# Kernel tuning notes

Hardware: AMD Instinct MI355X
Metric: run time of the kernel (lower is better)

## Reference

```python
import jax, jax.numpy as jnp
import numpy as np

L, B, D = 4096, 4, 512  # seq_len, batch, embed_dim (nhead=1 so kdim=vdim=D)


def setup_inputs() -> dict:
    key = jax.random.key(0)
    ks = jax.random.split(key, 11)
    sc = 1.0 / np.sqrt(D)
    return {
        "x": jax.random.normal(ks[0], (L, B, D), jnp.float32),
        "e": jax.random.normal(ks[1], (L, B, D), jnp.float32),
        "relay": jax.random.normal(ks[2], (1, B, D), jnp.float32),
        "Wq": jax.random.normal(ks[3], (D, D), jnp.float32) * sc,
        "bq": jax.random.normal(ks[4], (D,), jnp.float32) * sc,
        "Wk": jax.random.normal(ks[5], (D, D), jnp.float32) * sc,
        "bk": jax.random.normal(ks[6], (D,), jnp.float32) * sc,
        "Wv": jax.random.normal(ks[7], (D, D), jnp.float32) * sc,
        "bv": jax.random.normal(ks[8], (D,), jnp.float32) * sc,
        "Wo": jax.random.normal(ks[9], (D, D), jnp.float32) * sc,
        "bo": jax.random.normal(ks[10], (D,), jnp.float32) * sc,
    }


def _window3(t):
    # t: [L,B,D] -> [L,B,3,D] with zero padding at the sequence boundaries
    # (matches nn.Unfold(kernel=[3,1], padding=[1,0]): positions l-1, l, l+1)
    n = t.shape[0]
    tp = jnp.pad(t, ((1, 1), (0, 0), (0, 0)))
    return jnp.stack([tp[:n], tp[1:n + 1], tp[2:n + 2]], axis=2)


def reference(x, e, relay, Wq, bq, Wk, bk, Wv, bv, Wo, bo):
    l, b, d = x.shape
    scale = 1.0 / jnp.sqrt(jnp.asarray(d, x.dtype))

    q = x @ Wq.T + bq          # [L,B,D]
    k = x @ Wk.T + bk
    v = x @ Wv.T + bv

    # cores = [embedding tokens e ; relay broadcast over L]  -> [2,L,B,D]
    s = jnp.broadcast_to(relay, (l, b, d))
    cores = jnp.stack([e, s], axis=0)
    k_c = cores @ Wk.T + bk    # [2,L,B,D]
    v_c = cores @ Wv.T + bv

    # ring (local windowed) attention: window = [k_{l-1},k_l,k_{l+1}, k(e_l), k(relay)]
    kw = jnp.concatenate([_window3(k), jnp.transpose(k_c, (1, 2, 0, 3))], axis=2)  # [L,B,5,D]
    vw = jnp.concatenate([_window3(v), jnp.transpose(v_c, (1, 2, 0, 3))], axis=2)  # [L,B,5,D]
    logits = jnp.einsum('lbd,lbwd->lbw', q, kw) * scale
    alphas = jax.nn.softmax(logits, axis=2)
    ring = jnp.einsum('lbw,lbwd->lbd', alphas, vw)  # [L,B,D]

    # star (relay) attention: query is the UNprojected relay token (as in source)
    k_r = relay @ Wk.T + bk    # [1,B,D]
    v_r = relay @ Wv.T + bv
    kk = jnp.concatenate([k, k_r], axis=0)  # [L+1,B,D]
    vv = jnp.concatenate([v, v_r], axis=0)
    s_logits = jnp.einsum('obd,nbd->bon', relay, kk) * scale  # [B,1,L+1]
    s_alphas = jax.nn.softmax(s_logits, axis=-1)
    star = jnp.einsum('bon,nbd->obd', s_alphas, vv)  # [1,B,D]

    return (ring @ Wo.T + bo, star @ Wo.T + bo)
```

## Files before the change

### kernel.cpp

```cpp
#include <hip/hip_runtime.h>
#include <hip/hip_fp16.h>

#define L_SEQ 4096
#define BATCH 4
#define DIM 512
#define M_ROWS (L_SEQ * BATCH)
#define SCALE 0.04419417382415922f
#define SLS 4097

typedef __attribute__((ext_vector_type(4))) float f32x4;
typedef __attribute__((ext_vector_type(8))) _Float16 f16x8;
typedef __attribute__((ext_vector_type(4))) _Float16 f16x4;

__device__ inline void gload16(const void* g, void* l) {
    __builtin_amdgcn_global_load_lds(
        (const __attribute__((address_space(1))) void*)g,
        (__attribute__((address_space(3))) void*)l, 16, 0, 0);
}

__device__ inline float wred_sum(float s) {
#pragma unroll
    for (int o = 32; o; o >>= 1) s += __shfl_xor(s, o);
    return s;
}
__device__ inline float wred_max(float s) {
#pragma unroll
    for (int o = 32; o; o >>= 1) s = fmaxf(s, __shfl_xor(s, o));
    return s;
}

__global__ __launch_bounds__(256) void prep(
    const float* __restrict__ x, const float* __restrict__ e,
    const float* __restrict__ Wq, const float* __restrict__ Wk,
    const float* __restrict__ Wv, const float* __restrict__ Wo,
    const float* __restrict__ bq, const float* __restrict__ bk, const float* __restrict__ bv,
    const float* __restrict__ relay,
    _Float16* __restrict__ xh, _Float16* __restrict__ eh,
    _Float16* __restrict__ Wqkv, _Float16* __restrict__ Wof, float* __restrict__ bqkv,
    float* __restrict__ krvr, float* __restrict__ star)
{
    const int bid = blockIdx.x;
    if (bid < 16384) {
        size_t i = (size_t)bid * 256 + threadIdx.x;
        const size_t NV = (size_t)M_ROWS * DIM / 4;
        const float* src; _Float16* dst; size_t j;
        if (i < NV) { src = x; dst = xh; j = i; } else { src = e; dst = eh; j = i - NV; }
        float4 v = ((const float4*)src)[j];
        f16x4 h = { (_Float16)v.x, (_Float16)v.y, (_Float16)v.z, (_Float16)v.w };
        ((f16x4*)dst)[j] = h;
    } else if (bid < 19456) {
        int i = (bid - 16384) * 256 + threadIdx.x;
        {
            int r = i >> 9, c = i & 511;
            const float* W = (r < 512) ? Wq : (r < 1024 ? Wk : Wv);
            Wqkv[i] = (_Float16)W[(size_t)(r & 511) * 512 + c];
        }
        if (i < 512 * 512) Wof[i] = (_Float16)Wo[i];
        if (i < 1536) bqkv[i] = (i < 512) ? bq[i] : (i < 1024 ? bk[i - 512] : bv[i - 1024]);
    } else {
        const int o = ((bid - 19456) << 2) + (threadIdx.x >> 6);
        const int lane = threadIdx.x & 63;
        const int sel = o >> 11, rem = o & 2047, b = rem >> 9, j = rem & 511;
        const float* W = sel ? Wv : Wk;
        const float* wr = W + (size_t)j * 512 + lane * 8;
        const float* rp = relay + (size_t)b * 512 + lane * 8;
        float4 w0 = *(const float4*)wr,  w1 = *(const float4*)(wr + 4);
        float4 r0 = *(const float4*)rp,  r1 = *(const float4*)(rp + 4);
        float s = w0.x * r0.x + w0.y * r0.y + w0.z * r0.z + w0.w * r0.w
                + w1.x * r1.x + w1.y * r1.y + w1.z * r1.z + w1.w * r1.w;
        s = wred_sum(s);
        if (lane == 0) {
            krvr[o] = s + (sel ? bv[j] : bk[j]);
            if (o < 2048) star[o] = 0.f;
        }
    }
}

template<int OUT16>
__global__ __launch_bounds__(256) void gemm_bt(
    const _Float16* __restrict__ A, const _Float16* __restrict__ Bm,
    const float* __restrict__ bias, void* __restrict__ Cv,
    int M, int N, int K)
{
    __shared__ _Float16 lA[2][128 * 32];
    __shared__ _Float16 lB[2][128 * 32];
    const int tid = threadIdx.x;
    const int wave = tid >> 6, lane = tid & 63;
    const int row0 = blockIdx.x * 128;
    const int col0 = blockIdx.y * 128;
    const int wm = (wave >> 1) * 64, wn = (wave & 1) * 64;

    f32x4 acc[4][4];
#pragma unroll
    for (int i = 0; i < 4; ++i)
#pragma unroll
        for (int j = 0; j < 4; ++j) acc[i][j] = (f32x4)0.f;

    const int idx0 = tid, idx1 = 256 + tid;
    const int r0_ = idx0 >> 2, c0_ = ((idx0 & 3) ^ ((idx0 >> 3) & 3)) * 8;
    const int r1_ = idx1 >> 2, c1_ = ((idx1 & 3) ^ ((idx1 >> 3) & 3)) * 8;
    const int ldsb0 = (wave * 64) * 8;
    const int ldsb1 = (256 + wave * 64) * 8;

    const int nsteps = K >> 5;
    auto stage = [&](int buf, int t) {
        const int k0 = t << 5;
        gload16(A  + (size_t)(row0 + r0_) * K + k0 + c0_, &lA[buf][ldsb0]);
        gload16(A  + (size_t)(row0 + r1_) * K + k0 + c1_, &lA[buf][ldsb1]);
        gload16(Bm + (size_t)(col0 + r0_) * K + k0 + c0_, &lB[buf][ldsb0]);
        gload16(Bm + (size_t)(col0 + r1_) * K + k0 + c1_, &lB[buf][ldsb1]);
    };
    stage(0, 0);
    stage(1, 1);

    const int rslot = ((lane >> 4) ^ ((lane >> 1) & 3)) * 8;
    const int arb = (wm + (lane & 15)) * 32 + rslot;
    const int brb = (wn + (lane & 15)) * 32 + rslot;

    int cur = 0;
    for (int t = 0; t < nsteps; ++t) {
        if (t + 1 < nsteps) asm volatile("s_waitcnt vmcnt(4)" ::: "memory");
        else                asm volatile("s_waitcnt vmcnt(0)" ::: "memory");
        __builtin_amdgcn_s_barrier();
        f16x8 af[4], bfr[4];
#pragma unroll
        for (int i = 0; i < 4; ++i) af[i]  = *(const f16x8*)(&lA[cur][arb + i * 512]);
#pragma unroll
        for (int i = 0; i < 4; ++i) bfr[i] = *(const f16x8*)(&lB[cur][brb + i * 512]);
        __builtin_amdgcn_s_setprio(1);
#pragma unroll
        for (int mi = 0; mi < 4; ++mi)
#pragma unroll
            for (int ni = 0; ni < 4; ++ni)
                acc[mi][ni] = __builtin_amdgcn_mfma_f32_16x16x32_f16(
                    af[mi], bfr[ni], acc[mi][ni], 0, 0, 0);
        __builtin_amdgcn_s_setprio(0);
        asm volatile("s_waitcnt lgkmcnt(0)" ::: "memory");
        __builtin_amdgcn_s_barrier();
        if (t + 2 < nsteps) stage(cur, t + 2);
        cur ^= 1;
    }

#pragma unroll
    for (int mi = 0; mi < 4; ++mi) {
#pragma unroll
        for (int ni = 0; ni < 4; ++ni) {
            const int col = col0 + wn + ni * 16 + (lane & 15);
            const float bb = bias[col];
#pragma unroll
            for (int r = 0; r < 4; ++r) {
                const int row = row0 + wm + mi * 16 + (lane >> 4) * 4 + r;
                float v = acc[mi][ni][r] + bb;
                if (OUT16) ((_Float16*)Cv)[(size_t)row * N + col] = (_Float16)v;
                else       ((float*)Cv)[(size_t)row * N + col] = v;
            }
        }
    }
}

__global__ __launch_bounds__(256) void ring_attn(
    const _Float16* __restrict__ qkv,
    const _Float16* __restrict__ ekv,
    const float* __restrict__ krvr,
    const float* __restrict__ relay,
    _Float16* __restrict__ ring,
    float* __restrict__ slog)
{
    const int wid = (blockIdx.x << 2) + (threadIdx.x >> 6);
    const int lane = threadIdx.x & 63;
    const int r = wid, b = r & 3, l = r >> 2;
    const int d0 = lane << 3;

    float q[8], rl[8];
    {
        f16x8 t = *(const f16x8*)(qkv + (size_t)r * 1536 + d0);
#pragma unroll
        for (int i = 0; i < 8; ++i) q[i] = (float)t[i];
        const float* rp = relay + (size_t)b * 512 + d0;
        float4 a = *(const float4*)rp, c = *(const float4*)(rp + 4);
        rl[0] = a.x; rl[1] = a.y; rl[2] = a.z; rl[3] = a.w;
        rl[4] = c.x; rl[5] = c.y; rl[6] = c.z; rl[7] = c.w;
    }
    const bool has0 = (l > 0), has2 = (l < L_SEQ - 1);

    auto dotk = [&](const _Float16* kp) -> float {
        f16x8 t = *(const f16x8*)(kp + d0);
        float s = 0.f;
#pragma unroll
        for (int i = 0; i < 8; ++i) s += q[i] * (float)t[i];
        return wred_sum(s);
    };

    float lg[5];
    lg[0] = has0 ? dotk(qkv + (size_t)(r - 4) * 1536 + 512) : 0.f;
    lg[2] = has2 ? dotk(qkv + (size_t)(r + 4) * 1536 + 512) : 0.f;
    lg[3] = dotk(ekv + (size_t)r * 1024);
    {
        f16x8 t = *(const f16x8*)(qkv + (size_t)r * 1536 + 512 + d0);
        float s1 = 0.f, s2 = 0.f;
#pragma unroll
        for (int i = 0; i < 8; ++i) { float kf = (float)t[i]; s1 += q[i] * kf; s2 += rl[i] * kf; }
#pragma unroll
        for (int o = 32; o; o >>= 1) { s1 += __shfl_xor(s1, o); s2 += __shfl_xor(s2, o); }
        lg[1] = s1;
        if (lane == 0) slog[(size_t)b * SLS + l] = s2 * SCALE;
    }
    {
        const float* kp = krvr + (size_t)b * 512 + d0;
        float s = 0.f;
#pragma unroll
        for (int i = 0; i < 8; ++i) s += q[i] * kp[i];
        lg[4] = wred_sum(s);
    }

    float li[5], m = -1e30f;
#pragma unroll
    for (int w = 0; w < 5; ++w) { li[w] = lg[w] * SCALE; m = fmaxf(m, li[w]); }
    float ew[5], Z = 0.f;
#pragma unroll
    for (int w = 0; w < 5; ++w) { ew[w] = expf(li[w] - m); Z += ew[w]; }
    const float inv = 1.f / Z;

    float o8[8] = {0, 0, 0, 0, 0, 0, 0, 0};
    auto addv = [&](const _Float16* vp, float a) {
        f16x8 t = *(const f16x8*)(vp + d0);
#pragma unroll
        for (int i = 0; i < 8; ++i) o8[i] += a * (float)t[i];
    };
    if (has0) addv(qkv + (size_t)(r - 4) * 1536 + 1024, ew[0] * inv);
    addv(qkv + (size_t)r * 1536 + 1024, ew[1] * inv);
    if (has2) addv(qkv + (size_t)(r + 4) * 1536 + 1024, ew[2] * inv);
    addv(ekv + (size_t)r * 1024 + 512, ew[3] * inv);
    {
        const float* vp = krvr + 2048 + (size_t)b * 512 + d0;
        const float a = ew[4] * inv;
#pragma unroll
        for (int i = 0; i < 8; ++i) o8[i] += a * vp[i];
    }
    f16x8 res;
#pragma unroll
    for (int i = 0; i < 8; ++i) res[i] = (_Float16)o8[i];
    *(f16x8*)(ring + (size_t)r * 512 + d0) = res;
}

__global__ __launch_bounds__(1024) void star_softmax(
    const float* __restrict__ relay, const float* __restrict__ krvr,
    float* __restrict__ slog)
{
    const int b = blockIdx.x, t = threadIdx.x, lane = t & 63, w = t >> 6;
    __shared__ float red[16];
    __shared__ float bc[2];
    float* sl = slog + (size_t)b * SLS;

    float p = 0.f;
    if (t < 512) p = relay[(size_t)b * 512 + t] * krvr[(size_t)b * 512 + t];
    p = wred_sum(p);
    if (lane == 0) red[w] = p;
    __syncthreads();
    if (t == 0) { float s = 0.f; for (int i = 0; i < 16; ++i) s += red[i]; bc[0] = s * SCALE; }
    __syncthreads();
    const float selfl = bc[0];
    __syncthreads();

    float v[4];
#pragma unroll
    for (int i = 0; i < 4; ++i) v[i] = sl[t + i * 1024];

    float m = selfl;
#pragma unroll
    for (int i = 0; i < 4; ++i) m = fmaxf(m, v[i]);
    m = wred_max(m);
    if (lane == 0) red[w] = m;
    __syncthreads();
    if (t == 0) { float mm = red[0]; for (int i = 1; i < 16; ++i) mm = fmaxf(mm, red[i]); bc[1] = mm; }
    __syncthreads();
    m = bc[1];

    float ev[4], z = (t == 0) ? expf(selfl - m) : 0.f;
#pragma unroll
    for (int i = 0; i < 4; ++i) { ev[i] = expf(v[i] - m); z += ev[i]; }
    z = wred_sum(z);
    if (lane == 0) red[w] = z;
    __syncthreads();
    if (t == 0) { float s = 0.f; for (int i = 0; i < 16; ++i) s += red[i]; bc[0] = 1.f / s; }
    __syncthreads();
    const float inv = bc[0];

#pragma unroll
    for (int i = 0; i < 4; ++i) sl[t + i * 1024] = ev[i] * inv;
    if (t == 0) sl[SLS - 1] = expf(selfl - m) * inv;
}

__global__ __launch_bounds__(256) void star_out(
    const float* __restrict__ slog, const _Float16* __restrict__ qkv,
    const float* __restrict__ krvr, float* __restrict__ star)
{
    const int b = threadIdx.x >> 6, lane = threadIdx.x & 63;
    const int chunk = blockIdx.x;
    const int d0 = lane << 3;
    const float* al = slog + (size_t)b * SLS;
    float acc[8] = {0, 0, 0, 0, 0, 0, 0, 0};
#pragma unroll 4
    for (int i = 0; i < 64; ++i) {
        const int n = chunk * 64 + i;
        const float a = al[n];
        f16x8 v = *(const f16x8*)(qkv + (size_t)(n * 4 + b) * 1536 + 1024 + d0);
#pragma unroll
        for (int j = 0; j < 8; ++j) acc[j] += a * (float)v[j];
    }
    if (chunk == 63) {
        const float a = al[SLS - 1];
        const float* vr = krvr + 2048 + (size_t)b * 512 + d0;
#pragma unroll
        for (int j = 0; j < 8; ++j) acc[j] += a * vr[j];
    }
#pragma unroll
    for (int j = 0; j < 8; ++j) atomicAdd(&star[(size_t)b * 512 + d0 + j], acc[j]);
}

__global__ __launch_bounds__(256) void star_proj(
    const float* __restrict__ star, const float* __restrict__ Wo,
    const float* __restrict__ bo, float* __restrict__ out1)
{
    const int o = (blockIdx.x << 2) + (threadIdx.x >> 6);
    const int lane = threadIdx.x & 63;
    const int b = o >> 9, j = o & 511;
    const float* sp = star + (size_t)b * 512 + lane * 8;
    const float* wr = Wo + (size_t)j * 512 + lane * 8;
    float4 w0 = *(const float4*)wr,  w1 = *(const float4*)(wr + 4);
    float4 s0 = *(const float4*)sp,  s1 = *(const float4*)(sp + 4);
    float s = w0.x * s0.x + w0.y * s0.y + w0.z * s0.z + w0.w * s0.w
            + w1.x * s1.x + w1.y * s1.y + w1.z * s1.z + w1.w * s1.w;
    s = wred_sum(s);
    if (lane == 0) out1[o] = s + bo[j];
}

extern "C" void kernel_launch(void* const* d_in, const int* in_sizes, int n_in,
                              void* d_out, int out_size, void* d_ws, size_t ws_size,
                              hipStream_t stream) {
    const float* x     = (const float*)d_in[0];
    const float* e     = (const float*)d_in[1];
    const float* relay = (const float*)d_in[2];
    const float* Wq    = (const float*)d_in[3];
    const float* bq    = (const float*)d_in[4];
    const float* Wk    = (const float*)d_in[5];
    const float* bk    = (const float*)d_in[6];
    const float* Wv    = (const float*)d_in[7];
    const float* bv    = (const float*)d_in[8];
    const float* Wo    = (const float*)d_in[9];
    const float* bo    = (const float*)d_in[10];
    float* out = (float*)d_out;

    size_t off = 0;
    auto alloc = [&](size_t bytes) {
        void* p = (char*)d_ws + off;
        off += (bytes + 255) & ~(size_t)255;
        return p;
    };
    _Float16* Wqkv = (_Float16*)alloc((size_t)1536 * 512 * 2);
    _Float16* Wof  = (_Float16*)alloc((size_t)512 * 512 * 2);
    float*    bqkv = (float*)   alloc(1536 * 4);
    _Float16* xh   = (_Float16*)alloc((size_t)M_ROWS * 512 * 2);
    _Float16* eh   = (_Float16*)alloc((size_t)M_ROWS * 512 * 2);
    _Float16* qkv  = (_Float16*)alloc((size_t)M_ROWS * 1536 * 2);
    _Float16* ekv  = (_Float16*)alloc((size_t)M_ROWS * 1024 * 2);
    float*    krvr = (float*)   alloc(2 * 4 * 512 * 4);
    float*    slog = (float*)   alloc((size_t)4 * SLS * 4);
    float*    star = (float*)   alloc(4 * 512 * 4);
    _Float16* ringb = xh;

    prep<<<16384 + 3072 + 1024, 256, 0, stream>>>(
        x, e, Wq, Wk, Wv, Wo, bq, bk, bv, relay,
        xh, eh, Wqkv, Wof, bqkv, krvr, star);

    gemm_bt<1><<<dim3(M_ROWS / 128, 1536 / 128), 256, 0, stream>>>(
        xh, Wqkv, bqkv, qkv, M_ROWS, 1536, 512);
    gemm_bt<1><<<dim3(M_ROWS / 128, 1024 / 128), 256, 0, stream>>>(
        eh, Wqkv + (size_t)512 * 512, bqkv + 512, ekv, M_ROWS, 1024, 512);

    ring_attn<<<M_ROWS / 4, 256, 0, stream>>>(qkv, ekv, krvr, relay, ringb, slog);

    star_softmax<<<4, 1024, 0, stream>>>(relay, krvr, slog);
    star_out<<<64, 256, 0, stream>>>(slog, qkv, krvr, star);

    gemm_bt<0><<<dim3(M_ROWS / 128, 512 / 128), 256, 0, stream>>>(
        ringb, Wof, bo, out, M_ROWS, 512, 512);
    star_proj<<<512, 256, 0, stream>>>(star, Wo, bo, out + (size_t)M_ROWS * 512);
}
```

Measured before the change: 160.8 us.

## Replace GEMMs with 256x256-tile 8-wave kernel, merging QKV and E-KV launches

Swaps the 128x128-tile, 4-wave GEMM for a 256x256-tile, 8-wave kernel with a 4-slot LDS pipeline that prefetches three K-steps ahead and splits the A and B loads around two MFMA half-passes. The x-QKV and e-KV projections now run as one launch, with a block-id swizzle over the combined tile space. The output projection uses the same kernel with only 128 blocks. The bigger tiles raise data reuse per block, at the cost of 64 KB of LDS and more registers, fewer resident blocks, and a possibly underfilled output GEMM.

```diff
diff --git a/kernel.cpp b/kernel.cpp
--- a/kernel.cpp
+++ b/kernel.cpp
@@ -76,83 +76,115 @@
     }
 }
 
+struct GemmP {
+    const _Float16* A;
+    const _Float16* W;
+    const float*    bias;
+    void*           C;
+    int             cstride;
+};
+
 template<int OUT16>
-__global__ __launch_bounds__(256) void gemm_bt(
-    const _Float16* __restrict__ A, const _Float16* __restrict__ Bm,
-    const float* __restrict__ bias, void* __restrict__ Cv,
-    int M, int N, int K)
-{
-    __shared__ _Float16 lA[2][128 * 32];
-    __shared__ _Float16 lB[2][128 * 32];
+__global__ __launch_bounds__(512) void gemm8p(GemmP g0, GemmP g1, int n0, int cpx)
+{
+    __shared__ _Float16 sA[4][256 * 32];
+    __shared__ _Float16 sB[4][256 * 32];
+
+    const int bid = blockIdx.x;
+    const int swz = (bid & 7) * cpx + (bid >> 3);
+    const GemmP g = (swz < n0) ? g0 : g1;
+    const int l  = (swz < n0) ? swz : swz - n0;
+    const int mt = l & 63, nt = l >> 6;
+    const int row0 = mt * 256;
+
     const int tid = threadIdx.x;
     const int wave = tid >> 6, lane = tid & 63;
-    const int row0 = blockIdx.x * 128;
-    const int col0 = blockIdx.y * 128;
-    const int wm = (wave >> 1) * 64, wn = (wave & 1) * 64;
-
-    f32x4 acc[4][4];
-#pragma unroll
-    for (int i = 0; i < 4; ++i)
+    const int wm = (wave >> 2) * 128, wn = (wave & 3) * 64;
+
+    const int sr0 = tid >> 2;
+    const int sc0 = ((tid & 3) ^ ((tid >> 3) & 3)) * 8;
+    const int ldsb0 = (wave * 64) * 8;
+    const int ldsb1 = (512 + wave * 64) * 8;
+
+    const _Float16* Abase = g.A + (size_t)row0 * 512;
+    const _Float16* Wbase = g.W + (size_t)(nt * 256) * 512;
+
+    auto stageA = [&](int slot, int s) {
+        const _Float16* src = Abase + s * 32;
+        gload16(src + (size_t)sr0 * 512 + sc0,         &sA[slot][ldsb0]);
+        gload16(src + (size_t)(sr0 + 128) * 512 + sc0, &sA[slot][ldsb1]);
+    };
+    auto stageB = [&](int slot, int s) {
+        const _Float16* src = Wbase + s * 32;
+        gload16(src + (size_t)sr0 * 512 + sc0,         &sB[slot][ldsb0]);
+        gload16(src + (size_t)(sr0 + 128) * 512 + sc0, &sB[slot][ldsb1]);
+    };
+
+    f32x4 acc[8][4];
+#pragma unroll
+    for (int i = 0; i < 8; ++i)
 #pragma unroll
         for (int j = 0; j < 4; ++j) acc[i][j] = (f32x4)0.f;
-
-    const int idx0 = tid, idx1 = 256 + tid;
-    const int r0_ = idx0 >> 2, c0_ = ((idx0 & 3) ^ ((idx0 >> 3) & 3)) * 8;
-    const int r1_ = idx1 >> 2, c1_ = ((idx1 & 3) ^ ((idx1 >> 3) & 3)) * 8;
-    const int ldsb0 = (wave * 64) * 8;
-    const int ldsb1 = (256 + wave * 64) * 8;
-
-    const int nsteps = K >> 5;
-    auto stage = [&](int buf, int t) {
-        const int k0 = t << 5;
-        gload16(A  + (size_t)(row0 + r0_) * K + k0 + c0_, &lA[buf][ldsb0]);
-        gload16(A  + (size_t)(row0 + r1_) * K + k0 + c1_, &lA[buf][ldsb1]);
-        gload16(Bm + (size_t)(col0 + r0_) * K + k0 + c0_, &lB[buf][ldsb0]);
-        gload16(Bm + (size_t)(col0 + r1_) * K + k0 + c1_, &lB[buf][ldsb1]);
-    };
-    stage(0, 0);
-    stage(1, 1);
 
     const int rslot = ((lane >> 4) ^ ((lane >> 1) & 3)) * 8;
     const int arb = (wm + (lane & 15)) * 32 + rslot;
     const int brb = (wn + (lane & 15)) * 32 + rslot;
 
-    int cur = 0;
-    for (int t = 0; t < nsteps; ++t) {
-        if (t + 1 < nsteps) asm volatile("s_waitcnt vmcnt(4)" ::: "memory");
-        else                asm volatile("s_waitcnt vmcnt(0)" ::: "memory");
-        __builtin_amdgcn_s_barrier();
-        f16x8 af[4], bfr[4];
-#pragma unroll
-        for (int i = 0; i < 4; ++i) af[i]  = *(const f16x8*)(&lA[cur][arb + i * 512]);
-#pragma unroll
-        for (int i = 0; i < 4; ++i) bfr[i] = *(const f16x8*)(&lB[cur][brb + i * 512]);
+    stageA(0, 0); stageB(0, 0);
+    stageA(1, 1); stageB(1, 1);
+    stageA(2, 2); stageB(2, 2);
+
+#pragma unroll 1
+    for (int s = 0; s < 16; ++s) {
+        const int rs = s & 3;
+        if (s <= 13)      asm volatile("s_waitcnt vmcnt(8)" ::: "memory");
+        else if (s == 14) asm volatile("s_waitcnt vmcnt(4)" ::: "memory");
+        else              asm volatile("s_waitcnt vmcnt(0)" ::: "memory");
+        asm volatile("s_barrier" ::: "memory");
+
+        if (s < 13) stageA((s + 3) & 3, s + 3);
+
+        const _Float16* pa = &sA[rs][0];
+        const _Float16* pb = &sB[rs][0];
+        f16x8 bf[4], af[4];
+#pragma unroll
+        for (int i = 0; i < 4; ++i) bf[i] = *(const f16x8*)(pb + brb + i * 512);
+#pragma unroll
+        for (int i = 0; i < 4; ++i) af[i] = *(const f16x8*)(pa + arb + i * 512);
         __builtin_amdgcn_s_setprio(1);
 #pragma unroll
         for (int mi = 0; mi < 4; ++mi)
 #pragma unroll
             for (int ni = 0; ni < 4; ++ni)
                 acc[mi][ni] = __builtin_amdgcn_mfma_f32_16x16x32_f16(
-                    af[mi], bfr[ni], acc[mi][ni], 0, 0, 0);
+                    af[mi], bf[ni], acc[mi][ni], 0, 0, 0);
         __builtin_amdgcn_s_setprio(0);
-        asm volatile("s_waitcnt lgkmcnt(0)" ::: "memory");
-        __builtin_amdgcn_s_barrier();
-        if (t + 2 < nsteps) stage(cur, t + 2);
-        cur ^= 1;
-    }
-
-#pragma unroll
-    for (int mi = 0; mi < 4; ++mi) {
-#pragma unroll
-        for (int ni = 0; ni < 4; ++ni) {
-            const int col = col0 + wn + ni * 16 + (lane & 15);
-            const float bb = bias[col];
+
+        if (s < 13) stageB((s + 3) & 3, s + 3);
+#pragma unroll
+        for (int i = 0; i < 4; ++i) af[i] = *(const f16x8*)(pa + arb + (i + 4) * 512);
+        __builtin_amdgcn_s_setprio(1);
+#pragma unroll
+        for (int mi = 0; mi < 4; ++mi)
+#pragma unroll
+            for (int ni = 0; ni < 4; ++ni)
+                acc[mi + 4][ni] = __builtin_amdgcn_mfma_f32_16x16x32_f16(
+                    af[mi], bf[ni], acc[mi + 4][ni], 0, 0, 0);
+        __builtin_amdgcn_s_setprio(0);
+    }
+
+#pragma unroll
+    for (int ni = 0; ni < 4; ++ni) {
+        const int col = nt * 256 + wn + ni * 16 + (lane & 15);
+        const float bb = g.bias[col];
+#pragma unroll
+        for (int mi = 0; mi < 8; ++mi) {
 #pragma unroll
             for (int r = 0; r < 4; ++r) {
                 const int row = row0 + wm + mi * 16 + (lane >> 4) * 4 + r;
                 float v = acc[mi][ni][r] + bb;
-                if (OUT16) ((_Float16*)Cv)[(size_t)row * N + col] = (_Float16)v;
-                else       ((float*)Cv)[(size_t)row * N + col] = v;
+                if (OUT16) ((_Float16*)g.C)[(size_t)row * g.cstride + col] = (_Float16)v;
+                else       ((float*)g.C)[(size_t)row * g.cstride + col] = v;
             }
         }
     }
@@ -373,17 +405,17 @@
         x, e, Wq, Wk, Wv, Wo, bq, bk, bv, relay,
         xh, eh, Wqkv, Wof, bqkv, krvr, star);
 
-    gemm_bt<1><<<dim3(M_ROWS / 128, 1536 / 128), 256, 0, stream>>>(
-        xh, Wqkv, bqkv, qkv, M_ROWS, 1536, 512);
-    gemm_bt<1><<<dim3(M_ROWS / 128, 1024 / 128), 256, 0, stream>>>(
-        eh, Wqkv + (size_t)512 * 512, bqkv + 512, ekv, M_ROWS, 1024, 512);
+    GemmP gq { xh, Wqkv,                      bqkv,       qkv, 1536 };
+    GemmP ge { eh, Wqkv + (size_t)512 * 512,  bqkv + 512, ekv, 1024 };
+    gemm8p<1><<<640, 512, 0, stream>>>(gq, ge, 384, 80);
 
     ring_attn<<<M_ROWS / 4, 256, 0, stream>>>(qkv, ekv, krvr, relay, ringb, slog);
 
     star_softmax<<<4, 1024, 0, stream>>>(relay, krvr, slog);
     star_out<<<64, 256, 0, stream>>>(slog, qkv, krvr, star);
 
-    gemm_bt<0><<<dim3(M_ROWS / 128, 512 / 128), 256, 0, stream>>>(
-        ringb, Wof, bo, out, M_ROWS, 512, 512);
+    GemmP go { ringb, Wof, bo, out, 512 };
+    gemm8p<0><<<128, 512, 0, stream>>>(go, go, 128, 16);
+
     star_proj<<<512, 256, 0, stream>>>(star, Wo, bo, out + (size_t)M_ROWS * 512);
 }
```

After: 178.8 us. 1.11x slower.

## Merge QKV and embedding GEMMs into one launch with XCD-aware block swizzle

Applied to the files above, without the earlier changes.

The x-QKV and e-KV projection GEMMs now run as a single grid launch that picks its problem per block, with a block-index swizzle that spreads tiles across the eight XCDs. The output-projection GEMM uses the same kernel. The fp32-to-fp16 prep kernel now converts 8 elements per thread and 4 weight elements per thread, cutting block count and using wider loads. The goal is to remove one launch and tail underutilisation and to improve L2 locality, at the cost of hardcoded K=512 and per-block dispatch logic.

```diff
diff --git a/kernel.cpp b/kernel.cpp
--- a/kernel.cpp
+++ b/kernel.cpp
@@ -29,6 +29,9 @@
     return s;
 }
 
+#define PREP_NV   1048576
+#define PREP_XE_B 8192
+#define PREP_W_B  768
 __global__ __launch_bounds__(256) void prep(
     const float* __restrict__ x, const float* __restrict__ e,
     const float* __restrict__ Wq, const float* __restrict__ Wk,
@@ -40,25 +43,28 @@
     float* __restrict__ krvr, float* __restrict__ star)
 {
     const int bid = blockIdx.x;
-    if (bid < 16384) {
-        size_t i = (size_t)bid * 256 + threadIdx.x;
-        const size_t NV = (size_t)M_ROWS * DIM / 4;
-        const float* src; _Float16* dst; size_t j;
-        if (i < NV) { src = x; dst = xh; j = i; } else { src = e; dst = eh; j = i - NV; }
-        float4 v = ((const float4*)src)[j];
-        f16x4 h = { (_Float16)v.x, (_Float16)v.y, (_Float16)v.z, (_Float16)v.w };
-        ((f16x4*)dst)[j] = h;
-    } else if (bid < 19456) {
-        int i = (bid - 16384) * 256 + threadIdx.x;
-        {
-            int r = i >> 9, c = i & 511;
-            const float* W = (r < 512) ? Wq : (r < 1024 ? Wk : Wv);
-            Wqkv[i] = (_Float16)W[(size_t)(r & 511) * 512 + c];
+    if (bid < PREP_XE_B) {
+        int j = bid * 256 + threadIdx.x;
+        const float* src; _Float16* dst;
+        if (j < PREP_NV) { src = x; dst = xh; } else { src = e; dst = eh; j -= PREP_NV; }
+        const float* p = src + (size_t)j * 8;
+        float4 a = *(const float4*)p, b = *(const float4*)(p + 4);
+        f16x8 h = { (_Float16)a.x, (_Float16)a.y, (_Float16)a.z, (_Float16)a.w,
+                    (_Float16)b.x, (_Float16)b.y, (_Float16)b.z, (_Float16)b.w };
+        *(f16x8*)(dst + (size_t)j * 8) = h;
+    } else if (bid < PREP_XE_B + PREP_W_B) {
+        const int w = (bid - PREP_XE_B) * 256 + threadIdx.x;
+        const int o = w * 4, r = o >> 9, c = o & 511;
+        const float* W = (r < 512) ? Wq : (r < 1024 ? Wk : Wv);
+        float4 v = *(const float4*)(W + (size_t)(r & 511) * 512 + c);
+        *(f16x4*)(Wqkv + o) = f16x4{ (_Float16)v.x, (_Float16)v.y, (_Float16)v.z, (_Float16)v.w };
+        if (o < 262144) {
+            float4 u = *(const float4*)(Wo + o);
+            *(f16x4*)(Wof + o) = f16x4{ (_Float16)u.x, (_Float16)u.y, (_Float16)u.z, (_Float16)u.w };
         }
-        if (i < 512 * 512) Wof[i] = (_Float16)Wo[i];
-        if (i < 1536) bqkv[i] = (i < 512) ? bq[i] : (i < 1024 ? bk[i - 512] : bv[i - 1024]);
+        if (w < 1536) bqkv[w] = (w < 512) ? bq[w] : (w < 1024 ? bk[w - 512] : bv[w - 1024]);
     } else {
-        const int o = ((bid - 19456) << 2) + (threadIdx.x >> 6);
+        const int o = ((bid - PREP_XE_B - PREP_W_B) << 2) + (threadIdx.x >> 6);
         const int lane = threadIdx.x & 63;
         const int sel = o >> 11, rem = o & 2047, b = rem >> 9, j = rem & 511;
         const float* W = sel ? Wv : Wk;
@@ -76,18 +82,29 @@
     }
 }
 
+struct GemmP {
+    const _Float16* A;
+    const _Float16* W;
+    const float*    bias;
+    void*           C;
+    int             cstride;
+    int             ncols;
+};
+
 template<int OUT16>
-__global__ __launch_bounds__(256) void gemm_bt(
-    const _Float16* __restrict__ A, const _Float16* __restrict__ Bm,
-    const float* __restrict__ bias, void* __restrict__ Cv,
-    int M, int N, int K)
+__global__ __launch_bounds__(256) void gemm2p(GemmP g0, GemmP g1, int n0, int cpx)
 {
     __shared__ _Float16 lA[2][128 * 32];
     __shared__ _Float16 lB[2][128 * 32];
+    const int bid = blockIdx.x;
+    const int swz = (bid & 7) * cpx + (bid >> 3);
+    const GemmP g = (swz < n0) ? g0 : g1;
+    const int l  = (swz < n0) ? swz : swz - n0;
+    const int mt = l / g.ncols, nt = l % g.ncols;
+    const int row0 = mt * 128, col0 = nt * 128;
+
     const int tid = threadIdx.x;
     const int wave = tid >> 6, lane = tid & 63;
-    const int row0 = blockIdx.x * 128;
-    const int col0 = blockIdx.y * 128;
     const int wm = (wave >> 1) * 64, wn = (wave & 1) * 64;
 
     f32x4 acc[4][4];
@@ -102,13 +119,12 @@
     const int ldsb0 = (wave * 64) * 8;
     const int ldsb1 = (256 + wave * 64) * 8;
 
-    const int nsteps = K >> 5;
     auto stage = [&](int buf, int t) {
         const int k0 = t << 5;
-        gload16(A  + (size_t)(row0 + r0_) * K + k0 + c0_, &lA[buf][ldsb0]);
-        gload16(A  + (size_t)(row0 + r1_) * K + k0 + c1_, &lA[buf][ldsb1]);
-        gload16(Bm + (size_t)(col0 + r0_) * K + k0 + c0_, &lB[buf][ldsb0]);
-        gload16(Bm + (size_t)(col0 + r1_) * K + k0 + c1_, &lB[buf][ldsb1]);
+        gload16(g.A + (size_t)(row0 + r0_) * 512 + k0 + c0_, &lA[buf][ldsb0]);
+        gload16(g.A + (size_t)(row0 + r1_) * 512 + k0 + c1_, &lA[buf][ldsb1]);
+        gload16(g.W + (size_t)(col0 + r0_) * 512 + k0 + c0_, &lB[buf][ldsb0]);
+        gload16(g.W + (size_t)(col0 + r1_) * 512 + k0 + c1_, &lB[buf][ldsb1]);
     };
     stage(0, 0);
     stage(1, 1);
@@ -118,9 +134,10 @@
     const int brb = (wn + (lane & 15)) * 32 + rslot;
 
     int cur = 0;
-    for (int t = 0; t < nsteps; ++t) {
-        if (t + 1 < nsteps) asm volatile("s_waitcnt vmcnt(4)" ::: "memory");
-        else                asm volatile("s_waitcnt vmcnt(0)" ::: "memory");
+#pragma unroll 1
+    for (int t = 0; t < 16; ++t) {
+        if (t + 1 < 16) asm volatile("s_waitcnt vmcnt(4)" ::: "memory");
+        else            asm volatile("s_waitcnt vmcnt(0)" ::: "memory");
         __builtin_amdgcn_s_barrier();
         f16x8 af[4], bfr[4];
 #pragma unroll
@@ -137,7 +154,7 @@
         __builtin_amdgcn_s_setprio(0);
         asm volatile("s_waitcnt lgkmcnt(0)" ::: "memory");
         __builtin_amdgcn_s_barrier();
-        if (t + 2 < nsteps) stage(cur, t + 2);
+        if (t + 2 < 16) stage(cur, t + 2);
         cur ^= 1;
     }
 
@@ -146,13 +163,13 @@
 #pragma unroll
         for (int ni = 0; ni < 4; ++ni) {
             const int col = col0 + wn + ni * 16 + (lane & 15);
-            const float bb = bias[col];
+            const float bb = g.bias[col];
 #pragma unroll
             for (int r = 0; r < 4; ++r) {
                 const int row = row0 + wm + mi * 16 + (lane >> 4) * 4 + r;
                 float v = acc[mi][ni][r] + bb;
-                if (OUT16) ((_Float16*)Cv)[(size_t)row * N + col] = (_Float16)v;
-                else       ((float*)Cv)[(size_t)row * N + col] = v;
+                if (OUT16) ((_Float16*)g.C)[(size_t)row * g.cstride + col] = (_Float16)v;
+                else       ((float*)g.C)[(size_t)row * g.cstride + col] = v;
             }
         }
     }
@@ -369,21 +386,21 @@
     float*    star = (float*)   alloc(4 * 512 * 4);
     _Float16* ringb = xh;
 
-    prep<<<16384 + 3072 + 1024, 256, 0, stream>>>(
+    prep<<<PREP_XE_B + PREP_W_B + 1024, 256, 0, stream>>>(
         x, e, Wq, Wk, Wv, Wo, bq, bk, bv, relay,
         xh, eh, Wqkv, Wof, bqkv, krvr, star);
 
-    gemm_bt<1><<<dim3(M_ROWS / 128, 1536 / 128), 256, 0, stream>>>(
-        xh, Wqkv, bqkv, qkv, M_ROWS, 1536, 512);
-    gemm_bt<1><<<dim3(M_ROWS / 128, 1024 / 128), 256, 0, stream>>>(
-        eh, Wqkv + (size_t)512 * 512, bqkv + 512, ekv, M_ROWS, 1024, 512);
+    GemmP gq { xh, Wqkv,                     bqkv,       qkv, 1536, 12 };
+    GemmP ge { eh, Wqkv + (size_t)512 * 512, bqkv + 512, ekv, 1024,  8 };
+    gemm2p<1><<<2560, 256, 0, stream>>>(gq, ge, 1536, 320);
 
     ring_attn<<<M_ROWS / 4, 256, 0, stream>>>(qkv, ekv, krvr, relay, ringb, slog);
 
     star_softmax<<<4, 1024, 0, stream>>>(relay, krvr, slog);
     star_out<<<64, 256, 0, stream>>>(slog, qkv, krvr, star);
 
-    gemm_bt<0><<<dim3(M_ROWS / 128, 512 / 128), 256, 0, stream>>>(
-        ringb, Wof, bo, out, M_ROWS, 512, 512);
+    GemmP go { ringb, Wof, bo, out, 512, 4 };
+    gemm2p<0><<<512, 256, 0, stream>>>(go, go, 512, 64);
+
     star_proj<<<512, 256, 0, stream>>>(star, Wo, bo, out + (size_t)M_ROWS * 512);
 }
```

New measurement: 156.6 us. -2.6%, faster.
